# Kernel tuning notes

Hardware: AMD Instinct MI355X
Metric: run time of the kernel (lower is better)

The kernel has to match this reference:

```python
import jax, jax.numpy as jnp
import numpy as np

B, T, C = 2, 2048, 2048
H, D, G = 16, 128, 4   # num_heads, head_dim, num_kv_groups
EPS = 1e-6


def setup_inputs() -> dict:
    key = jax.random.key(0)
    ks = jax.random.split(key, 6)
    x = jax.random.normal(ks[0], (B, T, C), dtype=jnp.float32)
    # causal mask: True = disallowed (strictly upper triangular)
    mask = jnp.triu(jnp.ones((T, T), dtype=bool), k=1)
    # RoPE tables, full head_dim with duplicated angle halves
    inv_freq = 1.0 / (10000.0 ** (jnp.arange(0, D, 2, dtype=jnp.float32) / D))
    angles = jnp.arange(T, dtype=jnp.float32)[:, None] * inv_freq[None, :]  # [T, D/2]
    angles = jnp.concatenate([angles, angles], axis=-1)                     # [T, D]
    cos, sin = jnp.cos(angles), jnp.sin(angles)
    std = 0.02
    W_query = jax.random.normal(ks[1], (C, H * D), dtype=jnp.float32) * std
    W_key = jax.random.normal(ks[2], (C, G * D), dtype=jnp.float32) * std
    W_value = jax.random.normal(ks[3], (C, G * D), dtype=jnp.float32) * std
    W_out = jax.random.normal(ks[4], (H * D, C), dtype=jnp.float32) * std
    q_scale = jnp.ones((D,), dtype=jnp.float32)
    k_scale = jnp.ones((D,), dtype=jnp.float32)
    return {"x": x, "mask": mask, "cos": cos, "sin": sin,
            "W_query": W_query, "W_key": W_key, "W_value": W_value,
            "W_out": W_out, "q_scale": q_scale, "k_scale": k_scale}


def _rmsnorm(x, scale):
    # qwen3-compatible: compute in fp32, rescale, cast back
    xf = x.astype(jnp.float32)
    var = jnp.mean(xf * xf, axis=-1, keepdims=True)
    return (xf * jax.lax.rsqrt(var + EPS) * scale).astype(x.dtype)


def _rope(x, cos, sin):
    d = x.shape[-1]
    x1, x2 = x[..., : d // 2], x[..., d // 2 :]
    rotated = jnp.concatenate([-x2, x1], axis=-1)
    # cos/sin: [T, D] -> broadcast over [B, H, T, D]
    return (x * cos[None, None] + rotated * sin[None, None]).astype(x.dtype)


def reference(x, mask, cos, sin, W_query, W_key, W_value, W_out, q_scale, k_scale):
    b, t, _ = x.shape
    Q = (x @ W_query).reshape(b, t, H, D).transpose(0, 2, 1, 3)  # [B,H,T,D]
    K = (x @ W_key).reshape(b, t, G, D).transpose(0, 2, 1, 3)    # [B,G,T,D]
    V = (x @ W_value).reshape(b, t, G, D).transpose(0, 2, 1, 3)
    group_size = H // G
    K = jnp.repeat(K, group_size, axis=1)  # [B,H,T,D]
    V = jnp.repeat(V, group_size, axis=1)
    Q = _rmsnorm(Q, q_scale)
    K = _rmsnorm(K, k_scale)
    Q = _rope(Q, cos, sin)
    K = _rope(K, cos, sin)
    scale = D ** (-0.5)
    attn = jnp.einsum("bhqd,bhkd->bhqk", Q, K) * scale
    attn = jnp.where(mask[None, None], -jnp.inf, attn)
    w = jax.nn.softmax(attn, axis=-1)
    out = jnp.einsum("bhqk,bhkd->bhqd", w, V)
    out = out.transpose(0, 2, 1, 3).reshape(b, t, H * D)
    return out @ W_out
```

## Files before the change

### kernel.cpp

```cpp
#include <hip/hip_runtime.h>
#include <hip/hip_bf16.h>

#define Bq 2
#define Tt 2048
#define Cc 2048
#define Hh 16
#define Dd 128
#define Gg 4

using bf16 = __hip_bfloat16;
typedef __attribute__((ext_vector_type(8))) short short8;
typedef __attribute__((ext_vector_type(4))) float f32x4;

__device__ __forceinline__ void gload_lds16(const void* g, void* l) {
    __builtin_amdgcn_global_load_lds(
        (const __attribute__((address_space(1))) unsigned int*)g,
        (__attribute__((address_space(3))) unsigned int*)l, 16, 0, 0);
}

__global__ void k_cast_bf16(const float* __restrict__ in, bf16* __restrict__ out, int n4) {
    int i = blockIdx.x * blockDim.x + threadIdx.x;
    if (i >= n4) return;
    float4 v = ((const float4*)in)[i];
    union { bf16 h[4]; uint2 u; } u;
    u.h[0] = __float2bfloat16(v.x);
    u.h[1] = __float2bfloat16(v.y);
    u.h[2] = __float2bfloat16(v.z);
    u.h[3] = __float2bfloat16(v.w);
    ((uint2*)out)[i] = u.u;
}

__global__ void k_cast_transpose(const float* __restrict__ in, bf16* __restrict__ out,
                                 int rows, int cols, int ostride) {
    __shared__ float tile[32][33];
    int c0 = blockIdx.x * 32, r0 = blockIdx.y * 32;
    int tx = threadIdx.x, ty = threadIdx.y;
    #pragma unroll
    for (int k = 0; k < 4; ++k)
        tile[ty + 8*k][tx] = in[(size_t)(r0 + ty + 8*k) * cols + c0 + tx];
    __syncthreads();
    #pragma unroll
    for (int k = 0; k < 4; ++k)
        out[(size_t)(c0 + ty + 8*k) * ostride + r0 + tx] = __float2bfloat16(tile[tx][ty + 8*k]);
}

__global__ void k_vt(const bf16* __restrict__ QKV, bf16* __restrict__ Vt) {
    __shared__ bf16 tile[64][65];
    const int d0 = blockIdx.x * 64, t0 = blockIdx.y * 64;
    const int bg = blockIdx.z;
    const int b = bg >> 2, g = bg & 3;
    const int tx = threadIdx.x, ty = threadIdx.y;
    const bf16* src = QKV + (size_t)(b * Tt) * 3072 + 2560 + g * 128;
    #pragma unroll
    for (int k = 0; k < 8; ++k)
        tile[ty + 8*k][tx] = src[(size_t)(t0 + ty + 8*k) * 3072 + d0 + tx];
    __syncthreads();
    bf16* dst = Vt + (size_t)bg * Dd * Tt;
    #pragma unroll
    for (int k = 0; k < 8; ++k)
        dst[(size_t)(d0 + ty + 8*k) * Tt + t0 + tx] = tile[tx][ty + 8*k];
}

template<int OUTF32>
__global__ __launch_bounds__(256)
void k_gemm_bt(const bf16* __restrict__ A, const bf16* __restrict__ Bt,
               void* __restrict__ C, int M, int N, int K) {
    __shared__ __align__(16) bf16 As[128 * 64];
    __shared__ __align__(16) bf16 Bs[128 * 64];
    const int lane = threadIdx.x & 63;
    const int wave = threadIdx.x >> 6;
    const int row0 = blockIdx.y * 128;
    const int col0 = blockIdx.x * 128;
    const int wm = wave >> 1, wn = wave & 1;
    f32x4 acc[4][4] = {};

    const int srow = lane >> 3;
    const int schunk = ((lane & 7) ^ srow) * 8;

    for (int k0 = 0; k0 < K; k0 += 64) {
        #pragma unroll
        for (int j = 0; j < 4; ++j) {
            const int c = j * 4 + wave;
            const int rt = c * 8 + srow;
            gload_lds16(A  + (size_t)(row0 + rt) * K + k0 + schunk, As + c * 512);
            gload_lds16(Bt + (size_t)(col0 + rt) * K + k0 + schunk, Bs + c * 512);
        }
        __syncthreads();
        #pragma unroll
        for (int kk = 0; kk < 2; ++kk) {
            short8 af[4], bfr[4];
            #pragma unroll
            for (int i = 0; i < 4; ++i) {
                const int ra = wm * 64 + i * 16 + (lane & 15);
                af[i] = *(const short8*)((const char*)As + ra * 128 +
                        ((kk * 64 + (lane >> 4) * 16) ^ ((ra & 7) << 4)));
                const int rb = wn * 64 + i * 16 + (lane & 15);
                bfr[i] = *(const short8*)((const char*)Bs + rb * 128 +
                        ((kk * 64 + (lane >> 4) * 16) ^ ((rb & 7) << 4)));
            }
            __builtin_amdgcn_s_setprio(1);
            #pragma unroll
            for (int i = 0; i < 4; ++i)
                #pragma unroll
                for (int j = 0; j < 4; ++j)
                    acc[i][j] = __builtin_amdgcn_mfma_f32_16x16x32_bf16(af[i], bfr[j], acc[i][j], 0, 0, 0);
            __builtin_amdgcn_s_setprio(0);
        }
        __syncthreads();
    }

    const int crow0 = row0 + wm * 64 + (lane >> 4) * 4;
    const int ccol0 = col0 + wn * 64 + (lane & 15);
    #pragma unroll
    for (int i = 0; i < 4; ++i)
        #pragma unroll
        for (int j = 0; j < 4; ++j)
            #pragma unroll
            for (int r = 0; r < 4; ++r) {
                const size_t idx = (size_t)(crow0 + i * 16 + r) * N + ccol0 + j * 16;
                const float v = acc[i][j][r];
                if (OUTF32) ((float*)C)[idx] = v;
                else        ((bf16*)C)[idx] = __float2bfloat16(v);
            }
}

__global__ void k_qkv_post(const bf16* __restrict__ QKV,
                           const float* __restrict__ cosT, const float* __restrict__ sinT,
                           const float* __restrict__ qs, const float* __restrict__ ks,
                           bf16* __restrict__ Qr, bf16* __restrict__ Kr) {
    const int bt = blockIdx.x;
    const int b = bt >> 11;
    const int t = bt & 2047;
    const int lane = threadIdx.x & 63;
    const int wave = threadIdx.x >> 6;
    const float c1 = cosT[t * 128 + lane],      c2 = cosT[t * 128 + 64 + lane];
    const float s1 = sinT[t * 128 + lane],      s2 = sinT[t * 128 + 64 + lane];
    const float qs1 = qs[lane], qs2 = qs[lane + 64];
    const float ks1 = ks[lane], ks2 = ks[lane + 64];
    const bf16* rowb = QKV + (size_t)bt * 3072;
    for (int rr = wave; rr < 20; rr += 4) {
        const bf16* src = rowb + rr * 128;
        const float x1 = __bfloat162float(src[lane]);
        const float x2 = __bfloat162float(src[lane + 64]);
        bf16* dst;
        if (rr < 16) dst = Qr + ((size_t)(b * Hh + rr) * Tt + t) * 128;
        else         dst = Kr + ((size_t)(b * Gg + (rr - 16)) * Tt + t) * 128;
        float ssum = x1 * x1 + x2 * x2;
        #pragma unroll
        for (int o = 32; o > 0; o >>= 1) ssum += __shfl_xor(ssum, o);
        const float inv = rsqrtf(ssum * (1.0f / 128.0f) + 1e-6f);
        const float post = (rr < 16) ? 0.08838834764831845f : 1.0f;
        const float sc1 = ((rr < 16) ? qs1 : ks1) * inv;
        const float sc2 = ((rr < 16) ? qs2 : ks2) * inv;
        const float y1 = x1 * sc1;
        const float y2 = x2 * sc2;
        dst[lane]      = __float2bfloat16((y1 * c1 - y2 * s1) * post);
        dst[lane + 64] = __float2bfloat16((y2 * c2 + y1 * s2) * post);
    }
}

__global__ __launch_bounds__(256)
void k_attn(const bf16* __restrict__ Qr, const bf16* __restrict__ Kr,
            const bf16* __restrict__ Vt, bf16* __restrict__ AO) {
    __shared__ __align__(16) bf16 Ksm[2][64 * 128];
    __shared__ __align__(16) bf16 Vsm[2][128 * 64];
    __shared__ __align__(16) bf16 Psm[4][16 * 64];
    const int id = blockIdx.x;
    const int bg = id & 7;
    const int wid = id >> 3;
    const int pair = wid & 15;
    const int hg = wid >> 4;
    const int b = bg >> 2, g = bg & 3;
    const int h = g * 4 + hg;
    const int lane = threadIdx.x & 63;
    const int wave = threadIdx.x >> 6;

    const bf16* Kbase = Kr + (size_t)(b * Gg + g) * Tt * Dd;
    const bf16* Vbase = Vt + (size_t)(b * Gg + g) * Dd * Tt;

    for (int pass = 0; pass < 2; ++pass) {
        const int qt = pass ? (31 - pair) : pair;
        const bf16* Qbase = Qr + ((size_t)(b * Hh + h) * Tt + qt * 64) * Dd;

        short8 qf[4];
        #pragma unroll
        for (int kk = 0; kk < 4; ++kk)
            qf[kk] = *(const short8*)(Qbase + (size_t)(wave * 16 + (lane & 15)) * 128 + kk * 32 + (lane >> 4) * 8);

        float l_run[4] = {0.f, 0.f, 0.f, 0.f};
        f32x4 oacc[8];
        #pragma unroll
        for (int j = 0; j < 8; ++j) oacc[j] = (f32x4){0.f, 0.f, 0.f, 0.f};

        {
            #pragma unroll
            for (int j = 0; j < 4; ++j) {
                const int c = j * 4 + wave;
                const int rtk = c * 4 + (lane >> 4);
                const int chk = (lane & 15) ^ (rtk & 7);
                gload_lds16(Kbase + (size_t)rtk * 128 + chk * 8, Ksm[0] + c * 512);
                const int rtv = c * 8 + (lane >> 3);
                const int chv = (lane & 7) ^ ((lane >> 3) & 7);
                gload_lds16(Vbase + (size_t)rtv * Tt + chv * 8, Vsm[0] + c * 512);
            }
        }

        int cur = 0;
        for (int tk = 0; tk <= qt; ++tk) {
            __syncthreads();

            if (tk < qt) {
                const int k0n = (tk + 1) * 64;
                #pragma unroll
                for (int j = 0; j < 4; ++j) {
                    const int c = j * 4 + wave;
                    const int rtk = c * 4 + (lane >> 4);
                    const int chk = (lane & 15) ^ (rtk & 7);
                    gload_lds16(Kbase + (size_t)(k0n + rtk) * 128 + chk * 8, Ksm[cur ^ 1] + c * 512);
                    const int rtv = c * 8 + (lane >> 3);
                    const int chv = (lane & 7) ^ ((lane >> 3) & 7);
                    gload_lds16(Vbase + (size_t)rtv * Tt + k0n + chv * 8, Vsm[cur ^ 1] + c * 512);
                }
            }

            const bf16* Ks = Ksm[cur];
            const bf16* Vs = Vsm[cur];

            f32x4 s[4];
            #pragma unroll
            for (int nt = 0; nt < 4; ++nt) s[nt] = (f32x4){0.f, 0.f, 0.f, 0.f};
            __builtin_amdgcn_s_setprio(1);
            #pragma unroll
            for (int nt = 0; nt < 4; ++nt) {
                #pragma unroll
                for (int kk = 0; kk < 4; ++kk) {
                    const int rk = nt * 16 + (lane & 15);
                    short8 kf = *(const short8*)((const char*)Ks + rk * 256 +
                                ((kk * 64 + (lane >> 4) * 16) ^ ((rk & 7) << 4)));
                    s[nt] = __builtin_amdgcn_mfma_f32_16x16x32_bf16(qf[kk], kf, s[nt], 0, 0, 0);
                }
            }
            __builtin_amdgcn_s_setprio(0);

            if (tk == qt) {
                const int qrow = qt * 64 + wave * 16 + (lane >> 4) * 4;
                const int k0 = tk * 64;
                #pragma unroll
                for (int nt = 0; nt < 4; ++nt) {
                    const int kcol = k0 + nt * 16 + (lane & 15);
                    #pragma unroll
                    for (int r = 0; r < 4; ++r)
                        if (kcol > qrow + r) s[nt][r] = -1e30f;
                }
            }

            #pragma unroll
            for (int nt = 0; nt < 4; ++nt)
                #pragma unroll
                for (int r = 0; r < 4; ++r) {
                    const float p = __expf(s[nt][r]);
                    l_run[r] += p;
                    s[nt][r] = p;
                }

            #pragma unroll
            for (int nt = 0; nt < 4; ++nt)
                #pragma unroll
                for (int r = 0; r < 4; ++r) {
                    const int prow = (lane >> 4) * 4 + r;
                    const int pcol = nt * 16 + (lane & 15);
                    *(bf16*)((char*)Psm[wave] + ((prow * 128 + pcol * 2) ^ ((prow & 7) << 4))) =
                        __float2bfloat16(s[nt][r]);
                }
            #pragma unroll
            for (int kk = 0; kk < 2; ++kk) {
                const int pr = lane & 15;
                short8 pf = *(const short8*)((const char*)Psm[wave] + pr * 128 +
                            ((kk * 64 + (lane >> 4) * 16) ^ ((pr & 7) << 4)));
                __builtin_amdgcn_s_setprio(1);
                #pragma unroll
                for (int j = 0; j < 8; ++j) {
                    const int rb = j * 16 + (lane & 15);
                    short8 vf = *(const short8*)((const char*)Vs + rb * 128 +
                                ((kk * 64 + (lane >> 4) * 16) ^ ((rb & 7) << 4)));
                    oacc[j] = __builtin_amdgcn_mfma_f32_16x16x32_bf16(pf, vf, oacc[j], 0, 0, 0);
                }
                __builtin_amdgcn_s_setprio(0);
            }
            cur ^= 1;
        }
        __syncthreads();

        #pragma unroll
        for (int o = 1; o < 16; o <<= 1)
            #pragma unroll
            for (int r = 0; r < 4; ++r) l_run[r] += __shfl_xor(l_run[r], o);

        #pragma unroll
        for (int r = 0; r < 4; ++r) {
            const float inv = 1.0f / l_run[r];
            const int qrow = qt * 64 + wave * 16 + (lane >> 4) * 4 + r;
            bf16* dst = AO + (size_t)(b * Tt + qrow) * 2048 + h * 128 + (lane & 15);
            #pragma unroll
            for (int j = 0; j < 8; ++j)
                dst[j * 16] = __float2bfloat16(oacc[j][r] * inv);
        }
    }
}

extern "C" void kernel_launch(void* const* d_in, const int* in_sizes, int n_in,
                              void* d_out, int out_size, void* d_ws, size_t ws_size,
                              hipStream_t stream) {
    const float* x    = (const float*)d_in[0];
    const float* cosT = (const float*)d_in[2];
    const float* sinT = (const float*)d_in[3];
    const float* Wq   = (const float*)d_in[4];
    const float* Wk   = (const float*)d_in[5];
    const float* Wv   = (const float*)d_in[6];
    const float* Wo   = (const float*)d_in[7];
    const float* qs   = (const float*)d_in[8];
    const float* ks   = (const float*)d_in[9];

    char* ws = (char*)d_ws;
    bf16* xb   = (bf16*)(ws);
    bf16* Wcat = (bf16*)(ws + 16777216);
    bf16* Wot  = (bf16*)(ws + 29360128);
    bf16* QKV  = (bf16*)(ws + 37748736);
    bf16* Qr   = (bf16*)(ws + 62914560);
    bf16* Kr   = (bf16*)(ws + 79691776);
    bf16* Vtp  = (bf16*)(ws + 83886080);
    bf16* AO   = (bf16*)(ws + 88080384);

    k_cast_bf16<<<8192, 256, 0, stream>>>(x, xb, 2097152);
    dim3 tb(32, 8);
    k_cast_transpose<<<dim3(64, 64), tb, 0, stream>>>(Wq, Wcat, 2048, 2048, 2048);
    k_cast_transpose<<<dim3(16, 64), tb, 0, stream>>>(Wk, Wcat + (size_t)2048 * 2048, 2048, 512, 2048);
    k_cast_transpose<<<dim3(16, 64), tb, 0, stream>>>(Wv, Wcat + (size_t)2560 * 2048, 2048, 512, 2048);
    k_cast_transpose<<<dim3(64, 64), tb, 0, stream>>>(Wo, Wot, 2048, 2048, 2048);

    k_gemm_bt<0><<<dim3(24, 32), 256, 0, stream>>>(xb, Wcat, QKV, 4096, 3072, 2048);
    k_qkv_post<<<4096, 256, 0, stream>>>(QKV, cosT, sinT, qs, ks, Qr, Kr);
    k_vt<<<dim3(2, 32, 8), dim3(64, 8), 0, stream>>>(QKV, Vtp);
    k_attn<<<512, 256, 0, stream>>>(Qr, Kr, Vtp, AO);
    k_gemm_bt<1><<<dim3(16, 32), 256, 0, stream>>>(AO, Wot, d_out, 4096, 2048, 2048);
}
```

Before: 199.3 us.

## Replace GEMM with 256x256-tile double-buffered 8-wave kernel with XCD-aware block swizzle

The 128x128 single-buffered bf16 GEMM is replaced by a 512-thread kernel that computes 256x256 output tiles. It double-buffers the A/B LDS tiles and spreads the next tile's global-to-LDS loads across the four MFMA phases, using explicit vmcnt waits and barriers. Block IDs are remapped so neighbouring tiles land on the same XCD for L2 reuse. The aim is to hide load latency and cut global traffic per FLOP. In exchange, the grids shrink to 192 and 128 blocks, and the 128 KB of LDS likely allows only one block per CU, which may leave CUs idle.

```diff
diff --git a/kernel.cpp b/kernel.cpp
--- a/kernel.cpp
+++ b/kernel.cpp
@@ -62,57 +62,169 @@
 }
 
 template<int OUTF32>
-__global__ __launch_bounds__(256)
-void k_gemm_bt(const bf16* __restrict__ A, const bf16* __restrict__ Bt,
-               void* __restrict__ C, int M, int N, int K) {
-    __shared__ __align__(16) bf16 As[128 * 64];
-    __shared__ __align__(16) bf16 Bs[128 * 64];
-    const int lane = threadIdx.x & 63;
-    const int wave = threadIdx.x >> 6;
-    const int row0 = blockIdx.y * 128;
-    const int col0 = blockIdx.x * 128;
-    const int wm = wave >> 1, wn = wave & 1;
-    f32x4 acc[4][4] = {};
-
-    const int srow = lane >> 3;
-    const int schunk = ((lane & 7) ^ srow) * 8;
-
-    for (int k0 = 0; k0 < K; k0 += 64) {
-        #pragma unroll
-        for (int j = 0; j < 4; ++j) {
-            const int c = j * 4 + wave;
-            const int rt = c * 8 + srow;
-            gload_lds16(A  + (size_t)(row0 + rt) * K + k0 + schunk, As + c * 512);
-            gload_lds16(Bt + (size_t)(col0 + rt) * K + k0 + schunk, Bs + c * 512);
-        }
-        __syncthreads();
-        #pragma unroll
-        for (int kk = 0; kk < 2; ++kk) {
-            short8 af[4], bfr[4];
-            #pragma unroll
-            for (int i = 0; i < 4; ++i) {
-                const int ra = wm * 64 + i * 16 + (lane & 15);
-                af[i] = *(const short8*)((const char*)As + ra * 128 +
-                        ((kk * 64 + (lane >> 4) * 16) ^ ((ra & 7) << 4)));
-                const int rb = wn * 64 + i * 16 + (lane & 15);
-                bfr[i] = *(const short8*)((const char*)Bs + rb * 128 +
-                        ((kk * 64 + (lane >> 4) * 16) ^ ((rb & 7) << 4)));
-            }
+__global__ __launch_bounds__(512, 2)
+void k_gemm8(const bf16* __restrict__ A, const bf16* __restrict__ Bt,
+             void* __restrict__ C, int M, int N, int K, int nbx) {
+    __shared__ __align__(16) bf16 As[2][256 * 64];
+    __shared__ __align__(16) bf16 Bs[2][256 * 64];
+    const int tid = threadIdx.x;
+    const int lane = tid & 63;
+    const int wid = tid >> 6;
+    const int wm = wid >> 2, wn = wid & 3;
+
+    const int nb = gridDim.x;
+    const int cpx = nb >> 3;
+    const int id = blockIdx.x;
+    const int sid = (id & 7) * cpx + (id >> 3);
+    const int bx = sid % nbx, by = sid / nbx;
+    const int row0 = by * 256, col0 = bx * 256;
+
+    const int srow = tid >> 3;
+    const int NT = K >> 6;
+
+    f32x4 acc[8][4] = {};
+
+#define STAGE_A(bufq, tt, c) {                                              \
+        const int r_ = (c) * 64 + srow;                                     \
+        const int ch_ = (tid & 7) ^ (r_ & 7);                               \
+        gload_lds16(A + (size_t)(row0 + r_) * K + (tt) * 64 + ch_ * 8,      \
+                    &As[bufq][(c) * 4096 + wid * 512]); }
+#define STAGE_B(bufq, tt, c) {                                              \
+        const int r_ = (c) * 64 + srow;                                     \
+        const int ch_ = (tid & 7) ^ (r_ & 7);                               \
+        gload_lds16(Bt + (size_t)(col0 + r_) * K + (tt) * 64 + ch_ * 8,     \
+                    &Bs[bufq][(c) * 4096 + wid * 512]); }
+
+    #pragma unroll
+    for (int c = 0; c < 4; ++c) STAGE_A(0, 0, c);
+    #pragma unroll
+    for (int c = 0; c < 4; ++c) STAGE_B(0, 0, c);
+
+    for (int t = 0; t < NT; ++t) {
+        const int p = t & 1, q = p ^ 1;
+        const bf16* a = As[p];
+        const bf16* bm = Bs[p];
+        const bool pf = (t + 1 < NT);
+
+        auto rdA = [&](int i, int kk) -> short8 {
+            const int ra = wm * 128 + i * 16 + (lane & 15);
+            return *(const short8*)((const char*)a + ra * 128 +
+                   ((kk * 64 + (lane >> 4) * 16) ^ ((ra & 7) << 4)));
+        };
+        auto rdB = [&](int j, int kk) -> short8 {
+            const int rb = wn * 64 + j * 16 + (lane & 15);
+            return *(const short8*)((const char*)bm + rb * 128 +
+                   ((kk * 64 + (lane >> 4) * 16) ^ ((rb & 7) << 4)));
+        };
+
+        if (pf) { STAGE_A(q, t + 1, 0); STAGE_A(q, t + 1, 1); }
+        if (pf) asm volatile("s_waitcnt vmcnt(2)" ::: "memory");
+        else    asm volatile("s_waitcnt vmcnt(0)" ::: "memory");
+        __builtin_amdgcn_s_barrier();
+        asm volatile("" ::: "memory");
+
+        short8 af[4][2];
+        #pragma unroll
+        for (int i = 0; i < 4; ++i)
+            #pragma unroll
+            for (int kk = 0; kk < 2; ++kk) af[i][kk] = rdA(i, kk);
+        {
+            short8 bf0[2][2];
+            #pragma unroll
+            for (int j = 0; j < 2; ++j)
+                #pragma unroll
+                for (int kk = 0; kk < 2; ++kk) bf0[j][kk] = rdB(j, kk);
             __builtin_amdgcn_s_setprio(1);
             #pragma unroll
             for (int i = 0; i < 4; ++i)
                 #pragma unroll
-                for (int j = 0; j < 4; ++j)
-                    acc[i][j] = __builtin_amdgcn_mfma_f32_16x16x32_bf16(af[i], bfr[j], acc[i][j], 0, 0, 0);
+                for (int j = 0; j < 2; ++j)
+                    #pragma unroll
+                    for (int kk = 0; kk < 2; ++kk)
+                        acc[i][j] = __builtin_amdgcn_mfma_f32_16x16x32_bf16(af[i][kk], bf0[j][kk], acc[i][j], 0, 0, 0);
             __builtin_amdgcn_s_setprio(0);
         }
-        __syncthreads();
+        asm volatile("" ::: "memory");
+        __builtin_amdgcn_s_barrier();
+
+        {
+            short8 bf1[2][2];
+            #pragma unroll
+            for (int j = 0; j < 2; ++j)
+                #pragma unroll
+                for (int kk = 0; kk < 2; ++kk) bf1[j][kk] = rdB(j + 2, kk);
+            if (pf) { STAGE_A(q, t + 1, 2); STAGE_A(q, t + 1, 3); }
+            asm volatile("" ::: "memory");
+            __builtin_amdgcn_s_barrier();
+            __builtin_amdgcn_s_setprio(1);
+            #pragma unroll
+            for (int i = 0; i < 4; ++i)
+                #pragma unroll
+                for (int j = 0; j < 2; ++j)
+                    #pragma unroll
+                    for (int kk = 0; kk < 2; ++kk)
+                        acc[i][j + 2] = __builtin_amdgcn_mfma_f32_16x16x32_bf16(af[i][kk], bf1[j][kk], acc[i][j + 2], 0, 0, 0);
+            __builtin_amdgcn_s_setprio(0);
+        }
+        asm volatile("" ::: "memory");
+        __builtin_amdgcn_s_barrier();
+
+        short8 ag[4][2];
+        #pragma unroll
+        for (int i = 0; i < 4; ++i)
+            #pragma unroll
+            for (int kk = 0; kk < 2; ++kk) ag[i][kk] = rdA(i + 4, kk);
+        {
+            short8 bf0[2][2];
+            #pragma unroll
+            for (int j = 0; j < 2; ++j)
+                #pragma unroll
+                for (int kk = 0; kk < 2; ++kk) bf0[j][kk] = rdB(j, kk);
+            if (pf) { STAGE_B(q, t + 1, 0); STAGE_B(q, t + 1, 1); }
+            asm volatile("" ::: "memory");
+            __builtin_amdgcn_s_barrier();
+            __builtin_amdgcn_s_setprio(1);
+            #pragma unroll
+            for (int i = 0; i < 4; ++i)
+                #pragma unroll
+                for (int j = 0; j < 2; ++j)
+                    #pragma unroll
+                    for (int kk = 0; kk < 2; ++kk)
+                        acc[i + 4][j] = __builtin_amdgcn_mfma_f32_16x16x32_bf16(ag[i][kk], bf0[j][kk], acc[i + 4][j], 0, 0, 0);
+            __builtin_amdgcn_s_setprio(0);
+        }
+        asm volatile("" ::: "memory");
+        __builtin_amdgcn_s_barrier();
+
+        {
+            short8 bf1[2][2];
+            #pragma unroll
+            for (int j = 0; j < 2; ++j)
+                #pragma unroll
+                for (int kk = 0; kk < 2; ++kk) bf1[j][kk] = rdB(j + 2, kk);
+            if (pf) { STAGE_B(q, t + 1, 2); STAGE_B(q, t + 1, 3); }
+            asm volatile("" ::: "memory");
+            __builtin_amdgcn_s_barrier();
+            __builtin_amdgcn_s_setprio(1);
+            #pragma unroll
+            for (int i = 0; i < 4; ++i)
+                #pragma unroll
+                for (int j = 0; j < 2; ++j)
+                    #pragma unroll
+                    for (int kk = 0; kk < 2; ++kk)
+                        acc[i + 4][j + 2] = __builtin_amdgcn_mfma_f32_16x16x32_bf16(ag[i][kk], bf1[j][kk], acc[i + 4][j + 2], 0, 0, 0);
+            __builtin_amdgcn_s_setprio(0);
+        }
+        asm volatile("" ::: "memory");
+        __builtin_amdgcn_s_barrier();
     }
-
-    const int crow0 = row0 + wm * 64 + (lane >> 4) * 4;
+#undef STAGE_A
+#undef STAGE_B
+
+    const int crow0 = row0 + wm * 128 + (lane >> 4) * 4;
     const int ccol0 = col0 + wn * 64 + (lane & 15);
     #pragma unroll
-    for (int i = 0; i < 4; ++i)
+    for (int i = 0; i < 8; ++i)
         #pragma unroll
         for (int j = 0; j < 4; ++j)
             #pragma unroll
@@ -338,9 +450,9 @@
     k_cast_transpose<<<dim3(16, 64), tb, 0, stream>>>(Wv, Wcat + (size_t)2560 * 2048, 2048, 512, 2048);
     k_cast_transpose<<<dim3(64, 64), tb, 0, stream>>>(Wo, Wot, 2048, 2048, 2048);
 
-    k_gemm_bt<0><<<dim3(24, 32), 256, 0, stream>>>(xb, Wcat, QKV, 4096, 3072, 2048);
+    k_gemm8<0><<<192, 512, 0, stream>>>(xb, Wcat, QKV, 4096, 3072, 2048, 12);
     k_qkv_post<<<4096, 256, 0, stream>>>(QKV, cosT, sinT, qs, ks, Qr, Kr);
     k_vt<<<dim3(2, 32, 8), dim3(64, 8), 0, stream>>>(QKV, Vtp);
     k_attn<<<512, 256, 0, stream>>>(Qr, Kr, Vtp, AO);
-    k_gemm_bt<1><<<dim3(16, 32), 256, 0, stream>>>(AO, Wot, d_out, 4096, 2048, 2048);
-}
+    k_gemm8<1><<<128, 512, 0, stream>>>(AO, Wot, d_out, 4096, 2048, 2048, 8);
+}
```

Measured after the change: 237.0 us. 19.0% more time.

## Enlarge attention query tile to 128 rows so each wave reuses K/V fragments

Applied to the files above, without the earlier changes.

Each attention block now handles 128 query rows instead of 64. Each wave owns two 16-row sub-tiles and feeds every K and V fragment it loads from LDS into two MFMAs. The point is to halve the K/V global-to-LDS traffic and the LDS fragment reads per unit of attention work. The grid shrinks from 512 to 256 blocks, which is fewer than two waves of blocks on a 256-CU part, so occupancy and load balance suffer. Register pressure also rises from doubling the accumulators.

```diff
diff --git a/kernel.cpp b/kernel.cpp
--- a/kernel.cpp
+++ b/kernel.cpp
@@ -164,33 +164,41 @@
             const bf16* __restrict__ Vt, bf16* __restrict__ AO) {
     __shared__ __align__(16) bf16 Ksm[2][64 * 128];
     __shared__ __align__(16) bf16 Vsm[2][128 * 64];
-    __shared__ __align__(16) bf16 Psm[4][16 * 64];
+    __shared__ __align__(16) bf16 Psm[4][32 * 64];
     const int id = blockIdx.x;
     const int bg = id & 7;
     const int wid = id >> 3;
-    const int pair = wid & 15;
-    const int hg = wid >> 4;
+    const int pair = wid & 7;
+    const int hg = wid >> 3;
     const int b = bg >> 2, g = bg & 3;
     const int h = g * 4 + hg;
     const int lane = threadIdx.x & 63;
     const int wave = threadIdx.x >> 6;
+    const int hi = lane >> 4;
+    const int lq = lane & 15;
 
     const bf16* Kbase = Kr + (size_t)(b * Gg + g) * Tt * Dd;
     const bf16* Vbase = Vt + (size_t)(b * Gg + g) * Dd * Tt;
 
     for (int pass = 0; pass < 2; ++pass) {
-        const int qt = pass ? (31 - pair) : pair;
-        const bf16* Qbase = Qr + ((size_t)(b * Hh + h) * Tt + qt * 64) * Dd;
-
-        short8 qf[4];
-        #pragma unroll
-        for (int kk = 0; kk < 4; ++kk)
-            qf[kk] = *(const short8*)(Qbase + (size_t)(wave * 16 + (lane & 15)) * 128 + kk * 32 + (lane >> 4) * 8);
-
-        float l_run[4] = {0.f, 0.f, 0.f, 0.f};
-        f32x4 oacc[8];
-        #pragma unroll
-        for (int j = 0; j < 8; ++j) oacc[j] = (f32x4){0.f, 0.f, 0.f, 0.f};
+        const int qt = pass ? (15 - pair) : pair;
+        const int nkv = 2 * qt + 2;
+        const bf16* Qbase = Qr + ((size_t)(b * Hh + h) * Tt + qt * 128) * Dd;
+
+        short8 qf[2][4];
+        #pragma unroll
+        for (int sub = 0; sub < 2; ++sub)
+            #pragma unroll
+            for (int kk = 0; kk < 4; ++kk)
+                qf[sub][kk] = *(const short8*)(Qbase +
+                    (size_t)(wave * 32 + sub * 16 + lq) * 128 + kk * 32 + hi * 8);
+
+        float l_run[2][4] = {};
+        f32x4 oacc[2][8];
+        #pragma unroll
+        for (int sub = 0; sub < 2; ++sub)
+            #pragma unroll
+            for (int j = 0; j < 8; ++j) oacc[sub][j] = (f32x4){0.f, 0.f, 0.f, 0.f};
 
         {
             #pragma unroll
@@ -206,10 +214,10 @@
         }
 
         int cur = 0;
-        for (int tk = 0; tk <= qt; ++tk) {
+        for (int tk = 0; tk < nkv; ++tk) {
             __syncthreads();
 
-            if (tk < qt) {
+            if (tk + 1 < nkv) {
                 const int k0n = (tk + 1) * 64;
                 #pragma unroll
                 for (int j = 0; j < 4; ++j) {
@@ -226,64 +234,84 @@
             const bf16* Ks = Ksm[cur];
             const bf16* Vs = Vsm[cur];
 
-            f32x4 s[4];
-            #pragma unroll
-            for (int nt = 0; nt < 4; ++nt) s[nt] = (f32x4){0.f, 0.f, 0.f, 0.f};
-            __builtin_amdgcn_s_setprio(1);
+            f32x4 s[2][4];
+            #pragma unroll
+            for (int sub = 0; sub < 2; ++sub)
+                #pragma unroll
+                for (int nt = 0; nt < 4; ++nt) s[sub][nt] = (f32x4){0.f, 0.f, 0.f, 0.f};
             #pragma unroll
             for (int nt = 0; nt < 4; ++nt) {
-                #pragma unroll
-                for (int kk = 0; kk < 4; ++kk) {
-                    const int rk = nt * 16 + (lane & 15);
-                    short8 kf = *(const short8*)((const char*)Ks + rk * 256 +
-                                ((kk * 64 + (lane >> 4) * 16) ^ ((rk & 7) << 4)));
-                    s[nt] = __builtin_amdgcn_mfma_f32_16x16x32_bf16(qf[kk], kf, s[nt], 0, 0, 0);
+                const int rk = nt * 16 + lq;
+                short8 kf[4];
+                #pragma unroll
+                for (int kk = 0; kk < 4; ++kk)
+                    kf[kk] = *(const short8*)((const char*)Ks + rk * 256 +
+                             ((kk * 64 + hi * 16) ^ ((rk & 7) << 4)));
+                __builtin_amdgcn_s_setprio(1);
+                #pragma unroll
+                for (int sub = 0; sub < 2; ++sub)
+                    #pragma unroll
+                    for (int kk = 0; kk < 4; ++kk)
+                        s[sub][nt] = __builtin_amdgcn_mfma_f32_16x16x32_bf16(qf[sub][kk], kf[kk], s[sub][nt], 0, 0, 0);
+                __builtin_amdgcn_s_setprio(0);
+            }
+
+            if (tk >= nkv - 2) {
+                const int k0 = tk * 64;
+                #pragma unroll
+                for (int sub = 0; sub < 2; ++sub) {
+                    const int qrow = qt * 128 + wave * 32 + sub * 16 + hi * 4;
+                    #pragma unroll
+                    for (int nt = 0; nt < 4; ++nt) {
+                        const int kcol = k0 + nt * 16 + lq;
+                        #pragma unroll
+                        for (int r = 0; r < 4; ++r)
+                            if (kcol > qrow + r) s[sub][nt][r] = -1e30f;
+                    }
                 }
             }
-            __builtin_amdgcn_s_setprio(0);
-
-            if (tk == qt) {
-                const int qrow = qt * 64 + wave * 16 + (lane >> 4) * 4;
-                const int k0 = tk * 64;
-                #pragma unroll
-                for (int nt = 0; nt < 4; ++nt) {
-                    const int kcol = k0 + nt * 16 + (lane & 15);
-                    #pragma unroll
-                    for (int r = 0; r < 4; ++r)
-                        if (kcol > qrow + r) s[nt][r] = -1e30f;
+
+            #pragma unroll
+            for (int sub = 0; sub < 2; ++sub)
+                #pragma unroll
+                for (int nt = 0; nt < 4; ++nt)
+                    #pragma unroll
+                    for (int r = 0; r < 4; ++r) {
+                        const float p = __expf(s[sub][nt][r]);
+                        l_run[sub][r] += p;
+                        s[sub][nt][r] = p;
+                    }
+
+            #pragma unroll
+            for (int sub = 0; sub < 2; ++sub)
+                #pragma unroll
+                for (int nt = 0; nt < 4; ++nt)
+                    #pragma unroll
+                    for (int r = 0; r < 4; ++r) {
+                        const int prow = sub * 16 + hi * 4 + r;
+                        const int pcol = nt * 16 + lq;
+                        *(bf16*)((char*)Psm[wave] + ((prow * 128 + pcol * 2) ^ ((prow & 7) << 4))) =
+                            __float2bfloat16(s[sub][nt][r]);
+                    }
+
+            #pragma unroll
+            for (int kk = 0; kk < 2; ++kk) {
+                short8 pf[2];
+                #pragma unroll
+                for (int sub = 0; sub < 2; ++sub) {
+                    const int pr = sub * 16 + lq;
+                    pf[sub] = *(const short8*)((const char*)Psm[wave] + pr * 128 +
+                              ((kk * 64 + hi * 16) ^ ((pr & 7) << 4)));
                 }
-            }
-
-            #pragma unroll
-            for (int nt = 0; nt < 4; ++nt)
-                #pragma unroll
-                for (int r = 0; r < 4; ++r) {
-                    const float p = __expf(s[nt][r]);
-                    l_run[r] += p;
-                    s[nt][r] = p;
-                }
-
-            #pragma unroll
-            for (int nt = 0; nt < 4; ++nt)
-                #pragma unroll
-                for (int r = 0; r < 4; ++r) {
-                    const int prow = (lane >> 4) * 4 + r;
-                    const int pcol = nt * 16 + (lane & 15);
-                    *(bf16*)((char*)Psm[wave] + ((prow * 128 + pcol * 2) ^ ((prow & 7) << 4))) =
-                        __float2bfloat16(s[nt][r]);
-                }
-            #pragma unroll
-            for (int kk = 0; kk < 2; ++kk) {
-                const int pr = lane & 15;
-                short8 pf = *(const short8*)((const char*)Psm[wave] + pr * 128 +
-                            ((kk * 64 + (lane >> 4) * 16) ^ ((pr & 7) << 4)));
                 __builtin_amdgcn_s_setprio(1);
                 #pragma unroll
                 for (int j = 0; j < 8; ++j) {
-                    const int rb = j * 16 + (lane & 15);
+                    const int rb = j * 16 + lq;
                     short8 vf = *(const short8*)((const char*)Vs + rb * 128 +
-                                ((kk * 64 + (lane >> 4) * 16) ^ ((rb & 7) << 4)));
-                    oacc[j] = __builtin_amdgcn_mfma_f32_16x16x32_bf16(pf, vf, oacc[j], 0, 0, 0);
+                                ((kk * 64 + hi * 16) ^ ((rb & 7) << 4)));
+                    #pragma unroll
+                    for (int sub = 0; sub < 2; ++sub)
+                        oacc[sub][j] = __builtin_amdgcn_mfma_f32_16x16x32_bf16(pf[sub], vf, oacc[sub][j], 0, 0, 0);
                 }
                 __builtin_amdgcn_s_setprio(0);
             }
@@ -294,17 +322,21 @@
         #pragma unroll
         for (int o = 1; o < 16; o <<= 1)
             #pragma unroll
-            for (int r = 0; r < 4; ++r) l_run[r] += __shfl_xor(l_run[r], o);
-
-        #pragma unroll
-        for (int r = 0; r < 4; ++r) {
-            const float inv = 1.0f / l_run[r];
-            const int qrow = qt * 64 + wave * 16 + (lane >> 4) * 4 + r;
-            bf16* dst = AO + (size_t)(b * Tt + qrow) * 2048 + h * 128 + (lane & 15);
-            #pragma unroll
-            for (int j = 0; j < 8; ++j)
-                dst[j * 16] = __float2bfloat16(oacc[j][r] * inv);
-        }
+            for (int sub = 0; sub < 2; ++sub)
+                #pragma unroll
+                for (int r = 0; r < 4; ++r) l_run[sub][r] += __shfl_xor(l_run[sub][r], o);
+
+        #pragma unroll
+        for (int sub = 0; sub < 2; ++sub)
+            #pragma unroll
+            for (int r = 0; r < 4; ++r) {
+                const float inv = 1.0f / l_run[sub][r];
+                const int qrow = qt * 128 + wave * 32 + sub * 16 + hi * 4 + r;
+                bf16* dst = AO + (size_t)(b * Tt + qrow) * 2048 + h * 128 + lq;
+                #pragma unroll
+                for (int j = 0; j < 8; ++j)
+                    dst[j * 16] = __float2bfloat16(oacc[sub][j][r] * inv);
+            }
     }
 }
 
@@ -341,6 +373,6 @@
     k_gemm_bt<0><<<dim3(24, 32), 256, 0, stream>>>(xb, Wcat, QKV, 4096, 3072, 2048);
     k_qkv_post<<<4096, 256, 0, stream>>>(QKV, cosT, sinT, qs, ks, Qr, Kr);
     k_vt<<<dim3(2, 32, 8), dim3(64, 8), 0, stream>>>(QKV, Vtp);
-    k_attn<<<512, 256, 0, stream>>>(Qr, Kr, Vtp, AO);
+    k_attn<<<256, 256, 0, stream>>>(Qr, Kr, Vtp, AO);
     k_gemm_bt<1><<<dim3(16, 32), 256, 0, stream>>>(AO, Wot, d_out, 4096, 2048, 2048);
 }
```

New measurement: 211.5 us. +6.2%, slower.

## Restructure attention with 32x32 MFMA, register-resident P, and split-K wave pairs

Applied to the files above, without the earlier changes.

Rewrites the attention inner loop to use 32x32x16 bf16 MFMA, computing S transposed (K as A operand) so that P stays in registers. P is repacked into the PV operand layout with cvt_pk and cross-half lane shuffles instead of a round trip through LDS. Waves are split into two query sub-tiles, each with two key halves, and the key halves' partial outputs and row sums are combined through shared memory at the end. This removes the P LDS traffic and raises MFMA granularity, at the cost of an extra reduction step with two more barriers and larger accumulator register pressure.

```diff
diff --git a/kernel.cpp b/kernel.cpp
--- a/kernel.cpp
+++ b/kernel.cpp
@@ -11,11 +11,19 @@
 using bf16 = __hip_bfloat16;
 typedef __attribute__((ext_vector_type(8))) short short8;
 typedef __attribute__((ext_vector_type(4))) float f32x4;
+typedef __attribute__((ext_vector_type(16))) float f32x16;
+typedef unsigned int u32;
 
 __device__ __forceinline__ void gload_lds16(const void* g, void* l) {
     __builtin_amdgcn_global_load_lds(
         (const __attribute__((address_space(1))) unsigned int*)g,
         (__attribute__((address_space(3))) unsigned int*)l, 16, 0, 0);
+}
+
+__device__ __forceinline__ u32 cvtpk(float lo, float hi) {
+    u32 d;
+    asm("v_cvt_pk_bf16_f32 %0, %1, %2" : "=v"(d) : "v"(lo), "v"(hi));
+    return d;
 }
 
 __global__ void k_cast_bf16(const float* __restrict__ in, bf16* __restrict__ out, int n4) {
@@ -164,7 +172,6 @@
             const bf16* __restrict__ Vt, bf16* __restrict__ AO) {
     __shared__ __align__(16) bf16 Ksm[2][64 * 128];
     __shared__ __align__(16) bf16 Vsm[2][128 * 64];
-    __shared__ __align__(16) bf16 Psm[4][16 * 64];
     const int id = blockIdx.x;
     const int bg = id & 7;
     const int wid = id >> 3;
@@ -173,29 +180,33 @@
     const int b = bg >> 2, g = bg & 3;
     const int h = g * 4 + hg;
     const int lane = threadIdx.x & 63;
-    const int wave = threadIdx.x >> 6;
+    const int w = threadIdx.x >> 6;
+    const int qsub = w >> 1, khalf = w & 1;
+    const int l31 = lane & 31, hi32 = lane >> 5;
 
     const bf16* Kbase = Kr + (size_t)(b * Gg + g) * Tt * Dd;
     const bf16* Vbase = Vt + (size_t)(b * Gg + g) * Dd * Tt;
 
     for (int pass = 0; pass < 2; ++pass) {
         const int qt = pass ? (31 - pair) : pair;
-        const bf16* Qbase = Qr + ((size_t)(b * Hh + h) * Tt + qt * 64) * Dd;
-
-        short8 qf[4];
-        #pragma unroll
-        for (int kk = 0; kk < 4; ++kk)
-            qf[kk] = *(const short8*)(Qbase + (size_t)(wave * 16 + (lane & 15)) * 128 + kk * 32 + (lane >> 4) * 8);
-
-        float l_run[4] = {0.f, 0.f, 0.f, 0.f};
-        f32x4 oacc[8];
-        #pragma unroll
-        for (int j = 0; j < 8; ++j) oacc[j] = (f32x4){0.f, 0.f, 0.f, 0.f};
-
+        const int nkv = qt + 1;
+        const int qbase = qt * 64 + qsub * 32;
+
+        short8 qf[8];
         {
+            const bf16* Qp = Qr + ((size_t)(b * Hh + h) * Tt + qbase + l31) * 128;
+            #pragma unroll
+            for (int d = 0; d < 8; ++d)
+                qf[d] = *(const short8*)(Qp + d * 16 + hi32 * 8);
+        }
+
+        f32x16 oacc[4] = {};
+        float l_run = 0.f;
+
+        {
             #pragma unroll
             for (int j = 0; j < 4; ++j) {
-                const int c = j * 4 + wave;
+                const int c = j * 4 + w;
                 const int rtk = c * 4 + (lane >> 4);
                 const int chk = (lane & 15) ^ (rtk & 7);
                 gload_lds16(Kbase + (size_t)rtk * 128 + chk * 8, Ksm[0] + c * 512);
@@ -206,14 +217,14 @@
         }
 
         int cur = 0;
-        for (int tk = 0; tk <= qt; ++tk) {
+        for (int tk = 0; tk < nkv; ++tk) {
             __syncthreads();
 
-            if (tk < qt) {
+            if (tk + 1 < nkv) {
                 const int k0n = (tk + 1) * 64;
                 #pragma unroll
                 for (int j = 0; j < 4; ++j) {
-                    const int c = j * 4 + wave;
+                    const int c = j * 4 + w;
                     const int rtk = c * 4 + (lane >> 4);
                     const int chk = (lane & 15) ^ (rtk & 7);
                     gload_lds16(Kbase + (size_t)(k0n + rtk) * 128 + chk * 8, Ksm[cur ^ 1] + c * 512);
@@ -226,85 +237,107 @@
             const bf16* Ks = Ksm[cur];
             const bf16* Vs = Vsm[cur];
 
-            f32x4 s[4];
-            #pragma unroll
-            for (int nt = 0; nt < 4; ++nt) s[nt] = (f32x4){0.f, 0.f, 0.f, 0.f};
+            f32x16 sa = {}, sb = {};
+            const int krow = khalf * 32 + l31;
+            const int kbyte = krow * 256;
+            const int kswz = (krow & 7) << 4;
             __builtin_amdgcn_s_setprio(1);
             #pragma unroll
-            for (int nt = 0; nt < 4; ++nt) {
-                #pragma unroll
-                for (int kk = 0; kk < 4; ++kk) {
-                    const int rk = nt * 16 + (lane & 15);
-                    short8 kf = *(const short8*)((const char*)Ks + rk * 256 +
-                                ((kk * 64 + (lane >> 4) * 16) ^ ((rk & 7) << 4)));
-                    s[nt] = __builtin_amdgcn_mfma_f32_16x16x32_bf16(qf[kk], kf, s[nt], 0, 0, 0);
+            for (int d = 0; d < 4; ++d) {
+                short8 kf = *(const short8*)((const char*)Ks + kbyte + ((d * 32 + hi32 * 16) ^ kswz));
+                sa = __builtin_amdgcn_mfma_f32_32x32x16_bf16(kf, qf[d], sa, 0, 0, 0);
+            }
+            #pragma unroll
+            for (int d = 4; d < 8; ++d) {
+                short8 kf = *(const short8*)((const char*)Ks + kbyte + ((d * 32 + hi32 * 16) ^ kswz));
+                sb = __builtin_amdgcn_mfma_f32_32x32x16_bf16(kf, qf[d], sb, 0, 0, 0);
+            }
+            __builtin_amdgcn_s_setprio(0);
+
+            float p[16];
+            const int qrow_l = qbase + l31;
+            const int k0 = tk * 64 + khalf * 32;
+            #pragma unroll
+            for (int r = 0; r < 16; ++r) {
+                float v = sa[r] + sb[r];
+                if (tk == nkv - 1) {
+                    const int ktg = k0 + (r & 3) + 8 * (r >> 2) + 4 * hi32;
+                    if (ktg > qrow_l) v = -1e30f;
                 }
+                p[r] = __expf(v);
+                l_run += p[r];
+            }
+
+            short8 pa[2];
+            #pragma unroll
+            for (int s = 0; s < 2; ++s) {
+                const int bidx = s * 8;
+                u32 a0 = cvtpk(p[bidx + 0], p[bidx + 1]);
+                u32 a1 = cvtpk(p[bidx + 2], p[bidx + 3]);
+                u32 b0 = cvtpk(p[bidx + 4], p[bidx + 5]);
+                u32 b1 = cvtpk(p[bidx + 6], p[bidx + 7]);
+                u32 xa0 = (u32)__shfl_xor((int)a0, 32);
+                u32 xa1 = (u32)__shfl_xor((int)a1, 32);
+                u32 xb0 = (u32)__shfl_xor((int)b0, 32);
+                u32 xb1 = (u32)__shfl_xor((int)b1, 32);
+                union { u32 wq[4]; short8 s8; } uu;
+                uu.wq[0] = hi32 ? xb0 : a0;
+                uu.wq[1] = hi32 ? xb1 : a1;
+                uu.wq[2] = hi32 ? b0 : xa0;
+                uu.wq[3] = hi32 ? b1 : xa1;
+                pa[s] = uu.s8;
+            }
+
+            __builtin_amdgcn_s_setprio(1);
+            #pragma unroll
+            for (int db = 0; db < 4; ++db) {
+                const int vrow = db * 32 + l31;
+                const int vbyte = vrow * 128;
+                const int vswz = (vrow & 7) << 4;
+                #pragma unroll
+                for (int s = 0; s < 2; ++s) {
+                    short8 vf = *(const short8*)((const char*)Vs + vbyte +
+                                ((khalf * 64 + s * 32 + hi32 * 16) ^ vswz));
+                    oacc[db] = __builtin_amdgcn_mfma_f32_32x32x16_bf16(pa[s], vf, oacc[db], 0, 0, 0);
+                }
             }
             __builtin_amdgcn_s_setprio(0);
-
-            if (tk == qt) {
-                const int qrow = qt * 64 + wave * 16 + (lane >> 4) * 4;
-                const int k0 = tk * 64;
-                #pragma unroll
-                for (int nt = 0; nt < 4; ++nt) {
-                    const int kcol = k0 + nt * 16 + (lane & 15);
-                    #pragma unroll
-                    for (int r = 0; r < 4; ++r)
-                        if (kcol > qrow + r) s[nt][r] = -1e30f;
-                }
-            }
-
-            #pragma unroll
-            for (int nt = 0; nt < 4; ++nt)
-                #pragma unroll
-                for (int r = 0; r < 4; ++r) {
-                    const float p = __expf(s[nt][r]);
-                    l_run[r] += p;
-                    s[nt][r] = p;
-                }
-
-            #pragma unroll
-            for (int nt = 0; nt < 4; ++nt)
-                #pragma unroll
-                for (int r = 0; r < 4; ++r) {
-                    const int prow = (lane >> 4) * 4 + r;
-                    const int pcol = nt * 16 + (lane & 15);
-                    *(bf16*)((char*)Psm[wave] + ((prow * 128 + pcol * 2) ^ ((prow & 7) << 4))) =
-                        __float2bfloat16(s[nt][r]);
-                }
-            #pragma unroll
-            for (int kk = 0; kk < 2; ++kk) {
-                const int pr = lane & 15;
-                short8 pf = *(const short8*)((const char*)Psm[wave] + pr * 128 +
-                            ((kk * 64 + (lane >> 4) * 16) ^ ((pr & 7) << 4)));
-                __builtin_amdgcn_s_setprio(1);
-                #pragma unroll
-                for (int j = 0; j < 8; ++j) {
-                    const int rb = j * 16 + (lane & 15);
-                    short8 vf = *(const short8*)((const char*)Vs + rb * 128 +
-                                ((kk * 64 + (lane >> 4) * 16) ^ ((rb & 7) << 4)));
-                    oacc[j] = __builtin_amdgcn_mfma_f32_16x16x32_bf16(pf, vf, oacc[j], 0, 0, 0);
-                }
-                __builtin_amdgcn_s_setprio(0);
-            }
             cur ^= 1;
         }
-        __syncthreads();
-
-        #pragma unroll
-        for (int o = 1; o < 16; o <<= 1)
-            #pragma unroll
-            for (int r = 0; r < 4; ++r) l_run[r] += __shfl_xor(l_run[r], o);
-
-        #pragma unroll
-        for (int r = 0; r < 4; ++r) {
-            const float inv = 1.0f / l_run[r];
-            const int qrow = qt * 64 + wave * 16 + (lane >> 4) * 4 + r;
-            bf16* dst = AO + (size_t)(b * Tt + qrow) * 2048 + h * 128 + (lane & 15);
-            #pragma unroll
-            for (int j = 0; j < 8; ++j)
-                dst[j * 16] = __float2bfloat16(oacc[j][r] * inv);
-        }
+
+        __syncthreads();
+        float* scO = (float*)(&Ksm[0][0]);
+        float* scL = (float*)(&Vsm[0][0]);
+        if (khalf) {
+            #pragma unroll
+            for (int db = 0; db < 4; ++db)
+                #pragma unroll
+                for (int r = 0; r < 16; ++r)
+                    scO[qsub * 4096 + (db * 16 + r) * 64 + lane] = oacc[db][r];
+            scL[qsub * 64 + lane] = l_run;
+        }
+        __syncthreads();
+        if (!khalf) {
+            #pragma unroll
+            for (int db = 0; db < 4; ++db)
+                #pragma unroll
+                for (int r = 0; r < 16; ++r)
+                    oacc[db][r] += scO[qsub * 4096 + (db * 16 + r) * 64 + lane];
+            l_run += scL[qsub * 64 + lane];
+            l_run += __shfl_xor(l_run, 32);
+
+            #pragma unroll
+            for (int r = 0; r < 16; ++r) {
+                const int qr = (r & 3) + 8 * (r >> 2) + 4 * hi32;
+                const float linv = 1.0f / __shfl(l_run, qr);
+                const int qrow = qbase + qr;
+                bf16* dst = AO + ((size_t)(b * Tt) + qrow) * 2048 + h * 128 + l31;
+                #pragma unroll
+                for (int db = 0; db < 4; ++db)
+                    dst[db * 32] = __float2bfloat16(oacc[db][r] * linv);
+            }
+        }
+        __syncthreads();
     }
 }
 
```

Result: slower. 228.9 us (+14.9%).
